# Performance work log

Measured on AMD Instinct MI355X. Metric: run time of the kernel, lower is better.

Reference implementation:

```python
import jax, jax.numpy as jnp
import numpy as np

B, S, C, H = 2, 3144, 256, 8
HD = C // H                      # head_dim = key_dim = 32
SCALE = HD ** -0.5
QN = 8                           # queriesNum hard-coded in source
KS = 5                           # lepe depthwise conv kernel


def setup_inputs() -> dict:
    key = jax.random.key(0)
    ks = jax.random.split(key, 10)
    gain_qkv = 2 ** (-2.5) * (2.0 / (C + C)) ** 0.5  # xavier_normal std with gain 2^-2.5
    gain_out = (2.0 / (C + C)) ** 0.5
    return {
        "x": jax.random.normal(ks[0], (B, S, C), jnp.float32),
        "mask": jax.random.uniform(ks[1], (B, S, S), jnp.float32),
        "wq": jax.random.normal(ks[2], (C, C), jnp.float32) * gain_qkv,
        "bq": jnp.zeros((C,), jnp.float32),
        "wk": jax.random.normal(ks[3], (C, C), jnp.float32) * gain_qkv,
        "bk": jnp.zeros((C,), jnp.float32),
        "wv": jax.random.normal(ks[4], (C, C), jnp.float32) * gain_qkv,
        "bv": jnp.zeros((C,), jnp.float32),
        "lepe_w": jax.random.normal(ks[5], (KS, KS, 1, C), jnp.float32) * 0.05,  # depthwise HWIO
        "lepe_b": jnp.zeros((C,), jnp.float32),
        "wo": jax.random.normal(ks[6], (C, C), jnp.float32) * gain_out,
        "bo": jnp.zeros((C,), jnp.float32),
        "h": 56,
        "w": 56,
    }


def _dwconv(x_nhwc, kern, bias):
    # depthwise 5x5, stride 1, padding 2 (groups = channels)
    y = jax.lax.conv_general_dilated(
        x_nhwc, kern, window_strides=(1, 1), padding=((2, 2), (2, 2)),
        dimension_numbers=("NHWC", "HWIO", "NHWC"),
        feature_group_count=x_nhwc.shape[-1])
    return y + bias


def reference(x, mask, wq, bq, wk, bk, wv, bv, lepe_w, lepe_b, wo, bo, h, w):
    b, s, c = x.shape
    q = x @ wq.T + bq
    k = (x @ wk.T + bk) * SCALE
    v = x @ wv.T + bv
    # lepe positional residual on the non-query tokens
    lepe = _dwconv(v[:, QN:].reshape(b, h, w, c), lepe_w, lepe_b).reshape(b, h * w, c)
    qh = q.reshape(b, s, H, HD).transpose(0, 2, 1, 3)   # (b, H, s, hd)
    kh = k.reshape(b, s, H, HD).transpose(0, 2, 1, 3)
    vh = kh  # faithful to source: v_h = k.reshape(...)  (scaled k used as values)
    qk = jnp.einsum("bhqd,bhkd->bhqk", qh, kh)
    qk = qk + jnp.log(mask[:, None] + 1e-6)              # isSoftMask=True path
    attn = jax.nn.softmax(qk, axis=-1)
    out = jnp.einsum("bhqk,bhkd->bhqd", attn, vh)
    out = out.transpose(0, 2, 1, 3).reshape(b, s, c)
    out = out.at[:, QN:].add(lepe)
    return out @ wo.T + bo
```

## Files before the change

### kernel.cpp

```cpp
#include <hip/hip_runtime.h>


#define S_LEN 3144
#define SP    3200
#define HEADS 8
#define HD    32
#define BATCH 2
#define MROWS (BATCH*S_LEN)
#define NPIX  3136
#define SCALE_F 0.17677669529663687f

typedef __bf16 bf16x8  __attribute__((ext_vector_type(8)));
typedef __bf16 bf16x4  __attribute__((ext_vector_type(4)));
typedef float  floatx4 __attribute__((ext_vector_type(4)));
typedef short  shortx4 __attribute__((ext_vector_type(4)));

static __device__ __forceinline__ float bf2f(unsigned int h) {
  union { unsigned int u; float f; } v; v.u = h << 16; return v.f;
}
static __device__ __forceinline__ unsigned short f2bf(float f) {
  union { __bf16 b; unsigned short u; } v; v.b = (__bf16)f; return v.u;
}
static __device__ __forceinline__ bf16x8 ldcvt8(const float* __restrict__ p) {
  float4 a = *(const float4*)p;
  float4 b = *(const float4*)(p + 4);
  bf16x8 r;
  r[0]=(__bf16)a.x; r[1]=(__bf16)a.y; r[2]=(__bf16)a.z; r[3]=(__bf16)a.w;
  r[4]=(__bf16)b.x; r[5]=(__bf16)b.y; r[6]=(__bf16)b.z; r[7]=(__bf16)b.w;
  return r;
}

#define GLOBAL_AS __attribute__((address_space(1)))
#define LDS_AS    __attribute__((address_space(3)))
static __device__ __forceinline__ void gload_lds16(const void* g, void* l) {
  __builtin_amdgcn_global_load_lds((const GLOBAL_AS void*)g, (LDS_AS void*)l, 16, 0, 0);
}

__global__ __launch_bounds__(256) void k_qkv(
    const float* __restrict__ x,
    const float* __restrict__ wqp, const float* __restrict__ bqp,
    const float* __restrict__ wkp, const float* __restrict__ bkp,
    const float* __restrict__ wvp, const float* __restrict__ bvp,
    unsigned short* __restrict__ qws, unsigned short* __restrict__ kws,
    unsigned short* __restrict__ vfrag, unsigned short* __restrict__ vstage)
{
  __shared__ unsigned short lds_t[64 * 65];
  const int lane = threadIdx.x & 63;
  const int wid  = threadIdx.x >> 6;
  const int c    = lane & 15, quad = lane >> 4;
  const int bsel  = blockIdx.x / 50;
  const int stile = blockIdx.x % 50;
  const int srow0 = stile * 64;
  const int ncol = blockIdx.y * 64;
  const int wsel = ncol >> 8;
  const int col0 = ncol & 255;

  const float* wptr = (wsel == 0) ? wqp : (wsel == 1) ? wkp : wvp;
  const float* bptr = (wsel == 0) ? bqp : (wsel == 1) ? bkp : bvp;

  const int srow = srow0 + wid * 16 + c;
  const int arow = bsel * S_LEN + ((srow < S_LEN) ? srow : 0);
  const float* ap = x    + (size_t)arow * 256 + quad * 8;
  const float* bp = wptr + (size_t)(col0 + c) * 256 + quad * 8;

  floatx4 acc[4];
#pragma unroll
  for (int ct = 0; ct < 4; ++ct) acc[ct] = (floatx4){0.f, 0.f, 0.f, 0.f};

#pragma unroll
  for (int ks = 0; ks < 8; ++ks) {
    bf16x8 af = ldcvt8(ap + ks * 32);
#pragma unroll
    for (int ct = 0; ct < 4; ++ct) {
      bf16x8 bf = ldcvt8(bp + (size_t)ct * 16 * 256 + ks * 32);
      acc[ct] = __builtin_amdgcn_mfma_f32_16x16x32_bf16(af, bf, acc[ct], 0, 0, 0);
    }
  }

#pragma unroll
  for (int ct = 0; ct < 4; ++ct) {
    const int col = col0 + ct * 16 + c;
    const float bias = bptr[col];
#pragma unroll
    for (int r = 0; r < 4; ++r) {
      const int s = srow0 + quad * 4 + r + wid * 16;
      const int valid = (s < S_LEN);
      const float v = acc[ct][r] + bias;
      if (wsel == 0) {
        qws[(((size_t)(bsel * HEADS + (col >> 5))) * SP + s) * HD + (col & 31)] =
            valid ? f2bf(v) : (unsigned short)0;
      } else if (wsel == 1) {
        const unsigned short kb16 = valid ? f2bf(v * SCALE_F) : (unsigned short)0;
        kws[(((size_t)(bsel * HEADS + (col >> 5))) * SP + s) * HD + (col & 31)] = kb16;
        lds_t[(ct * 16 + c) * 65 + (wid * 16 + quad * 4 + r)] = kb16;
      } else {
        if (valid) vstage[(size_t)(bsel * S_LEN + s) * 256 + col] = f2bf(v);
      }
    }
  }

  if (wsel == 1) {
    __syncthreads();
    const int tid = threadIdx.x;
#pragma unroll
    for (int j = 0; j < 4; ++j) {
      const int grp  = j * 4 + (tid >> 6);
      const int l    = tid & 63;
      const int ct2  = grp & 3;
      const int half = (grp >> 2) & 1;
      const int hsel = grp >> 3;
      const int cc = l & 15, qq = l >> 4;
      const int cl = hsel * 32 + half * 16 + cc;
      const int rb = ct2 * 16 + qq * 4;
      union { shortx4 s4; unsigned short u[4]; } pk;
#pragma unroll
      for (int e = 0; e < 4; ++e) pk.u[e] = lds_t[cl * 65 + rb + e];
      const int hglob = (col0 >> 5) + hsel;
      const size_t off =
          ((((size_t)(bsel * HEADS + hglob) * 50 + stile) * 4 + ct2) * 2 + half) * 64 + l;
      *(shortx4*)(vfrag + off * 4) = pk.s4;
    }
  }
}

__global__ __launch_bounds__(256) void k_lepe(const unsigned short* __restrict__ vws,
                                              const float* __restrict__ cw,
                                              const float* __restrict__ cb,
                                              unsigned short* __restrict__ lepe)
{
  int idx = blockIdx.x * 256 + threadIdx.x;
  if (idx >= BATCH * NPIX * 32) return;
  const int cg = idx & 31;
  const int p  = (idx >> 5) % NPIX;
  const int b  = idx / (NPIX * 32);
  const int y  = p / 56, xx = p - y * 56;

  float acc[8];
  {
    float4 b0 = *(const float4*)(cb + cg * 8);
    float4 b1 = *(const float4*)(cb + cg * 8 + 4);
    acc[0]=b0.x; acc[1]=b0.y; acc[2]=b0.z; acc[3]=b0.w;
    acc[4]=b1.x; acc[5]=b1.y; acc[6]=b1.z; acc[7]=b1.w;
  }
#pragma unroll
  for (int dy = -2; dy <= 2; ++dy) {
    const int yy = y + dy;
    if ((unsigned)yy >= 56u) continue;
#pragma unroll
    for (int dx = -2; dx <= 2; ++dx) {
      const int xs = xx + dx;
      if ((unsigned)xs >= 56u) continue;
      uint4 vv = *(const uint4*)(vws + (size_t)(b * S_LEN + 8 + yy * 56 + xs) * 256 + cg * 8);
      const float* wp = cw + (size_t)((dy + 2) * 5 + (dx + 2)) * 256 + cg * 8;
      float4 w0 = *(const float4*)wp;
      float4 w1 = *(const float4*)(wp + 4);
      unsigned int va[4] = {vv.x, vv.y, vv.z, vv.w};
      acc[0] += bf2f(va[0] & 0xFFFFu) * w0.x;  acc[1] += bf2f(va[0] >> 16) * w0.y;
      acc[2] += bf2f(va[1] & 0xFFFFu) * w0.z;  acc[3] += bf2f(va[1] >> 16) * w0.w;
      acc[4] += bf2f(va[2] & 0xFFFFu) * w1.x;  acc[5] += bf2f(va[2] >> 16) * w1.y;
      acc[6] += bf2f(va[3] & 0xFFFFu) * w1.z;  acc[7] += bf2f(va[3] >> 16) * w1.w;
    }
  }
  unsigned int o[4];
#pragma unroll
  for (int j = 0; j < 4; ++j)
    o[j] = (unsigned int)f2bf(acc[2*j]) | ((unsigned int)f2bf(acc[2*j+1]) << 16);
  *((uint4*)(lepe + (size_t)(b * NPIX + p) * 256 + cg * 8)) = make_uint4(o[0], o[1], o[2], o[3]);
}

template<bool TAIL>
static __device__ __forceinline__ void proc_tile(
    int t, const unsigned short* __restrict__ kb,
    const unsigned short* __restrict__ vb,
    const float* __restrict__ mb,
    int c, int quad, int lane, const bf16x8 qf,
    floatx4& o0, floatx4& o1, float& l_run)
{
  const int k0 = t * 64;
  bf16x8 kf[4]; shortx4 v0[4], v1[4];
  const unsigned short* tb = vb + (size_t)t * 2048;
#pragma unroll
  for (int ct = 0; ct < 4; ++ct) {
    kf[ct] = *(const bf16x8*)(kb + (size_t)(k0 + ct * 16 + c) * HD + quad * 8);
    v0[ct] = *(const shortx4*)(tb + (ct * 2 + 0) * 256 + lane * 4);
    v1[ct] = *(const shortx4*)(tb + (ct * 2 + 1) * 256 + lane * 4);
  }
  floatx4 s[4];
#pragma unroll
  for (int ct = 0; ct < 4; ++ct)
    s[ct] = __builtin_amdgcn_mfma_f32_16x16x32_bf16(kf[ct], qf,
               (floatx4){0.f,0.f,0.f,0.f}, 0, 0, 0);
  float ls = 0.f;
  shortx4 pf[4];
#pragma unroll
  for (int ct = 0; ct < 4; ++ct) {
    const float4 mv = *(const float4*)(mb + c * 64 + (((ct * 4 + quad) ^ c) * 4));
    float pr[4];
    pr[0] = (mv.x + 1e-6f) * __expf(s[ct][0]);
    pr[1] = (mv.y + 1e-6f) * __expf(s[ct][1]);
    pr[2] = (mv.z + 1e-6f) * __expf(s[ct][2]);
    pr[3] = (mv.w + 1e-6f) * __expf(s[ct][3]);
    if (TAIL) {
      const int kk = k0 + ct * 16 + quad * 4;
#pragma unroll
      for (int r = 0; r < 4; ++r) if (kk + r >= S_LEN) pr[r] = 0.f;
    }
    ls += (pr[0] + pr[1]) + (pr[2] + pr[3]);
    union { bf16x4 b4; shortx4 s4; } u;
    u.b4[0]=(__bf16)pr[0]; u.b4[1]=(__bf16)pr[1]; u.b4[2]=(__bf16)pr[2]; u.b4[3]=(__bf16)pr[3];
    pf[ct] = u.s4;
  }
  l_run += ls;
#pragma unroll
  for (int ct = 0; ct < 4; ++ct) {
    o0 = __builtin_amdgcn_mfma_f32_16x16x16bf16_1k(v0[ct], pf[ct], o0, 0, 0, 0);
    o1 = __builtin_amdgcn_mfma_f32_16x16x16bf16_1k(v1[ct], pf[ct], o1, 0, 0, 0);
  }
}

__global__ __launch_bounds__(256) void k_flash(
    const unsigned short* __restrict__ qws,
    const unsigned short* __restrict__ kws,
    const unsigned short* __restrict__ vfrag,
    const float* __restrict__ mask,
    const unsigned short* __restrict__ lepe,
    unsigned short* __restrict__ attn)
{
  __shared__ __align__(16) float smem[4][2048];
  const int lane = threadIdx.x & 63;
  const int wid  = threadIdx.x >> 6;
  const int c    = lane & 15, quad = lane >> 4;
  const int u    = blockIdx.x;
  const int xcd  = u & 7;
  const int slot = u >> 3;
  const int h    = slot & 7;
  const int p    = (slot >> 3) * 8 + xcd;
  const int b    = p / 200;
  const int strip = p - b * 200;
  const int qrow = strip * 16 + c;
  const size_t bh = (size_t)(b * HEADS + h);

  const bf16x8 qf = *(const bf16x8*)(qws + (bh * SP + qrow) * HD + quad * 8);
  const unsigned short* kb = kws + bh * SP * HD;
  const unsigned short* vb = vfrag + bh * (size_t)(50 * 2048);
  float* mt = &smem[wid][0];

  const float* msrc[4];
  int goff4[4];
#pragma unroll
  for (int i = 0; i < 4; ++i) {
    const int rq = i * 4 + (lane >> 4);
    int mr = strip * 16 + rq; if (mr >= S_LEN) mr = S_LEN - 1;
    msrc[i] = mask + ((size_t)b * S_LEN + mr) * S_LEN;
    goff4[i] = ((lane & 15) ^ rq) * 4;
  }

  float l_run = 0.f;
  floatx4 o0 = (floatx4){0.f,0.f,0.f,0.f};
  floatx4 o1 = (floatx4){0.f,0.f,0.f,0.f};

  const int nt = (wid < 2) ? 13 : 12;

  {
    const int k0 = (wid * 12) * 64;
#pragma unroll
    for (int i = 0; i < 4; ++i)
      gload_lds16(msrc[i] + (k0 + goff4[i]), mt + i * 256);
  }

  for (int it = 0; it < nt; ++it) {
    const int t = (it < 12) ? wid * 12 + it : 48 + wid;
    if (it + 1 < nt) {
      const int tn = (it + 1 < 12) ? wid * 12 + it + 1 : 48 + wid;
      const int k0n = tn * 64;
      float* dst = mt + ((it + 1) & 1) * 1024;
      const bool tailn = (k0n + 63 >= S_LEN);
#pragma unroll
      for (int i = 0; i < 4; ++i) {
        int kk = k0n + goff4[i];
        if (tailn && kk > S_LEN - 4) kk = S_LEN - 4;
        gload_lds16(msrc[i] + kk, dst + i * 256);
      }
      asm volatile("s_waitcnt vmcnt(4)" ::: "memory");
    } else {
      asm volatile("s_waitcnt vmcnt(0)" ::: "memory");
    }
    const float* mb = mt + (it & 1) * 1024;
    if (wid == 1 && it == 12)
      proc_tile<true >(t, kb, vb, mb, c, quad, lane, qf, o0, o1, l_run);
    else
      proc_tile<false>(t, kb, vb, mb, c, quad, lane, qf, o0, o1, l_run);
  }

#pragma unroll
  for (int r = 0; r < 4; ++r) {
    smem[wid][lane * 9 + r]     = o0[r];
    smem[wid][lane * 9 + 4 + r] = o1[r];
  }
  smem[wid][lane * 9 + 8] = l_run;
  __syncthreads();

  if (wid == 0) {
#pragma unroll
    for (int w = 1; w < 4; ++w) {
#pragma unroll
      for (int r = 0; r < 4; ++r) {
        o0[r] += smem[w][lane * 9 + r];
        o1[r] += smem[w][lane * 9 + 4 + r];
      }
      l_run += smem[w][lane * 9 + 8];
    }
    l_run += __shfl_xor(l_run, 16);
    l_run += __shfl_xor(l_run, 32);
    const float rl = 1.f / l_run;

    if (qrow < S_LEN) {
      const size_t obase = ((size_t)b * S_LEN + qrow) * 256 + h * 32;
      const size_t lbase = (qrow >= 8) ? (((size_t)b * NPIX + (qrow - 8)) * 256 + h * 32) : 0;
#pragma unroll
      for (int mt2 = 0; mt2 < 2; ++mt2) {
        floatx4 ov = mt2 ? o1 : o0;
#pragma unroll
        for (int r = 0; r < 4; ++r) {
          const int d = mt2 * 16 + quad * 4 + r;
          float val = ov[r] * rl;
          if (qrow >= 8) val += bf2f(lepe[lbase + d]);
          attn[obase + d] = f2bf(val);
        }
      }
    }
  }
}

__global__ __launch_bounds__(256) void k_oproj(
    const unsigned short* __restrict__ attn,
    const float* __restrict__ wop,
    const float* __restrict__ bop,
    float* __restrict__ out)
{
  const int lane = threadIdx.x & 63;
  const int wid  = threadIdx.x >> 6;
  const int c = lane & 15, quad = lane >> 4;
  const int row0 = blockIdx.x * 64 + wid * 16;
  const int col0 = blockIdx.y * 64;

  int arow = row0 + c; if (arow >= MROWS) arow = 0;
  const unsigned short* ap = attn + (size_t)arow * 256 + quad * 8;
  const float* bp = wop + (size_t)(col0 + c) * 256 + quad * 8;

  floatx4 acc[4];
#pragma unroll
  for (int ct = 0; ct < 4; ++ct) acc[ct] = (floatx4){0.f,0.f,0.f,0.f};
#pragma unroll
  for (int ks = 0; ks < 8; ++ks) {
    bf16x8 af = *(const bf16x8*)(ap + ks * 32);
#pragma unroll
    for (int ct = 0; ct < 4; ++ct) {
      bf16x8 bf = ldcvt8(bp + (size_t)ct * 16 * 256 + ks * 32);
      acc[ct] = __builtin_amdgcn_mfma_f32_16x16x32_bf16(af, bf, acc[ct], 0, 0, 0);
    }
  }
#pragma unroll
  for (int ct = 0; ct < 4; ++ct) {
    const int col = col0 + ct * 16 + c;
    const float bias = bop[col];
#pragma unroll
    for (int r = 0; r < 4; ++r) {
      const int row = row0 + quad * 4 + r;
      if (row >= MROWS) continue;
      out[(size_t)row * 256 + col] = acc[ct][r] + bias;
    }
  }
}

#define QW_OFF 0u
#define KW_OFF 3276800u
#define VF_OFF 6553600u
#define LE_OFF 9830400u
#define AT_OFF 13041664u

extern "C" void kernel_launch(void* const* d_in, const int* in_sizes, int n_in,
                              void* d_out, int out_size, void* d_ws, size_t ws_size,
                              hipStream_t stream) {
  const float* x    = (const float*)d_in[0];
  const float* mask = (const float*)d_in[1];
  const float* wq   = (const float*)d_in[2];
  const float* bq   = (const float*)d_in[3];
  const float* wk   = (const float*)d_in[4];
  const float* bk   = (const float*)d_in[5];
  const float* wv   = (const float*)d_in[6];
  const float* bv   = (const float*)d_in[7];
  const float* lw   = (const float*)d_in[8];
  const float* lb   = (const float*)d_in[9];
  const float* wo   = (const float*)d_in[10];
  const float* bo   = (const float*)d_in[11];

  char* ws = (char*)d_ws;
  unsigned short* qws = (unsigned short*)(ws + QW_OFF);
  unsigned short* kws = (unsigned short*)(ws + KW_OFF);
  unsigned short* vfr = (unsigned short*)(ws + VF_OFF);
  unsigned short* lpe = (unsigned short*)(ws + LE_OFF);
  unsigned short* atb = (unsigned short*)(ws + AT_OFF);
  unsigned short* vst = (unsigned short*)d_out;
  float*          outf = (float*)d_out;

  k_qkv<<<dim3(100, 12), 256, 0, stream>>>(x, wq, bq, wk, bk, wv, bv, qws, kws, vfr, vst);
  k_lepe<<<784, 256, 0, stream>>>(vst, lw, lb, lpe);
  k_flash<<<3200, 256, 0, stream>>>(qws, kws, vfr, mask, lpe, atb);
  k_oproj<<<dim3(99, 4), 256, 0, stream>>>(atb, wo, bo, outf);
}
```

Baseline: 324.5 us.

## Pre-convert inputs to bf16, double-buffer K/V registers, use exp2 in flash

Adds a conversion kernel that turns x and the QKV weights into bf16 once, so the projection GEMM loads bf16 directly instead of converting fp32 on every load. The flash kernel now double-buffers K/V fragments in registers alongside the mask tiles in LDS, reads the mask with inline ds_read_b128 asm, and requests 3 blocks per SM through launch_bounds. The K used for scores is prescaled by log2(e) so the kernel can call the exp2 builtin. This adds a kernel launch, extra workspace aliasing into the output and LDS buffers, and higher register pressure.

After: 374.8 us. +15.5%, slower.

```diff
diff --git a/kernel.cpp b/kernel.cpp
--- a/kernel.cpp
+++ b/kernel.cpp
@@ -9,6 +9,7 @@
 #define MROWS (BATCH*S_LEN)
 #define NPIX  3136
 #define SCALE_F 0.17677669529663687f
+#define KQ_SC   0.25504472665352026f
 
 typedef __bf16 bf16x8  __attribute__((ext_vector_type(8)));
 typedef __bf16 bf16x4  __attribute__((ext_vector_type(4)));
@@ -36,11 +37,36 @@
   __builtin_amdgcn_global_load_lds((const GLOBAL_AS void*)g, (LDS_AS void*)l, 16, 0, 0);
 }
 
+#define FENCE16() asm volatile("s_waitcnt vmcnt(16)" ::: "memory")
+#define FENCE0()  asm volatile("s_waitcnt vmcnt(0)" ::: "memory")
+
+__global__ __launch_bounds__(256) void k_cvt(
+    const float* __restrict__ x, const float* __restrict__ wq,
+    const float* __restrict__ wk, const float* __restrict__ wv,
+    unsigned short* __restrict__ xb, unsigned short* __restrict__ w3b)
+{
+  const int i = blockIdx.x * 256 + threadIdx.x;
+  const int NX = MROWS * 32;
+  const int NW = 8192;
+  const float* src;
+  unsigned short* dst;
+  if (i < NX) { src = x + (size_t)i * 8; dst = xb + (size_t)i * 8; }
+  else {
+    const int j = i - NX;
+    if (j >= 3 * NW) return;
+    src = (j < NW) ? wq + (size_t)j * 8
+        : (j < 2 * NW) ? wk + (size_t)(j - NW) * 8
+                       : wv + (size_t)(j - 2 * NW) * 8;
+    dst = w3b + (size_t)j * 8;
+  }
+  bf16x8 v = ldcvt8(src);
+  *(bf16x8*)dst = v;
+}
+
 __global__ __launch_bounds__(256) void k_qkv(
-    const float* __restrict__ x,
-    const float* __restrict__ wqp, const float* __restrict__ bqp,
-    const float* __restrict__ wkp, const float* __restrict__ bkp,
-    const float* __restrict__ wvp, const float* __restrict__ bvp,
+    const unsigned short* __restrict__ xb, const unsigned short* __restrict__ w3b,
+    const float* __restrict__ bqp, const float* __restrict__ bkp,
+    const float* __restrict__ bvp,
     unsigned short* __restrict__ qws, unsigned short* __restrict__ kws,
     unsigned short* __restrict__ vfrag, unsigned short* __restrict__ vstage)
 {
@@ -55,13 +81,12 @@
   const int wsel = ncol >> 8;
   const int col0 = ncol & 255;
 
-  const float* wptr = (wsel == 0) ? wqp : (wsel == 1) ? wkp : wvp;
   const float* bptr = (wsel == 0) ? bqp : (wsel == 1) ? bkp : bvp;
 
   const int srow = srow0 + wid * 16 + c;
   const int arow = bsel * S_LEN + ((srow < S_LEN) ? srow : 0);
-  const float* ap = x    + (size_t)arow * 256 + quad * 8;
-  const float* bp = wptr + (size_t)(col0 + c) * 256 + quad * 8;
+  const unsigned short* ap = xb  + (size_t)arow * 256 + quad * 8;
+  const unsigned short* bp = w3b + (size_t)(ncol + c) * 256 + quad * 8;
 
   floatx4 acc[4];
 #pragma unroll
@@ -69,10 +94,10 @@
 
 #pragma unroll
   for (int ks = 0; ks < 8; ++ks) {
-    bf16x8 af = ldcvt8(ap + ks * 32);
+    bf16x8 af = *(const bf16x8*)(ap + ks * 32);
 #pragma unroll
     for (int ct = 0; ct < 4; ++ct) {
-      bf16x8 bf = ldcvt8(bp + (size_t)ct * 16 * 256 + ks * 32);
+      bf16x8 bf = *(const bf16x8*)(bp + (size_t)ct * 16 * 256 + ks * 32);
       acc[ct] = __builtin_amdgcn_mfma_f32_16x16x32_bf16(af, bf, acc[ct], 0, 0, 0);
     }
   }
@@ -83,16 +108,17 @@
     const float bias = bptr[col];
 #pragma unroll
     for (int r = 0; r < 4; ++r) {
-      const int s = srow0 + quad * 4 + r + wid * 16;
+      const int s = srow0 + wid * 16 + quad * 4 + r;
       const int valid = (s < S_LEN);
       const float v = acc[ct][r] + bias;
       if (wsel == 0) {
         qws[(((size_t)(bsel * HEADS + (col >> 5))) * SP + s) * HD + (col & 31)] =
             valid ? f2bf(v) : (unsigned short)0;
       } else if (wsel == 1) {
-        const unsigned short kb16 = valid ? f2bf(v * SCALE_F) : (unsigned short)0;
-        kws[(((size_t)(bsel * HEADS + (col >> 5))) * SP + s) * HD + (col & 31)] = kb16;
-        lds_t[(ct * 16 + c) * 65 + (wid * 16 + quad * 4 + r)] = kb16;
+        kws[(((size_t)(bsel * HEADS + (col >> 5))) * SP + s) * HD + (col & 31)] =
+            valid ? f2bf(v * KQ_SC) : (unsigned short)0;
+        lds_t[(ct * 16 + c) * 65 + (wid * 16 + quad * 4 + r)] =
+            valid ? f2bf(v * SCALE_F) : (unsigned short)0;
       } else {
         if (valid) vstage[(size_t)(bsel * S_LEN + s) * 256 + col] = f2bf(v);
       }
@@ -168,16 +194,26 @@
   *((uint4*)(lepe + (size_t)(b * NPIX + p) * 256 + cg * 8)) = make_uint4(o[0], o[1], o[2], o[3]);
 }
 
-template<bool TAIL>
-static __device__ __forceinline__ void proc_tile(
-    int t, const unsigned short* __restrict__ kb,
-    const unsigned short* __restrict__ vb,
-    const float* __restrict__ mb,
-    int c, int quad, int lane, const bf16x8 qf,
-    floatx4& o0, floatx4& o1, float& l_run)
+
+static __device__ __forceinline__ void ldsm4(
+    const unsigned (&ma)[4], floatx4& m0, floatx4& m1, floatx4& m2, floatx4& m3)
+{
+  asm volatile(
+      "ds_read_b128 %0, %4\n\t"
+      "ds_read_b128 %1, %5\n\t"
+      "ds_read_b128 %2, %6\n\t"
+      "ds_read_b128 %3, %7\n\t"
+      "s_waitcnt lgkmcnt(0)"
+      : "=v"(m0), "=v"(m1), "=v"(m2), "=v"(m3)
+      : "v"(ma[0]), "v"(ma[1]), "v"(ma[2]), "v"(ma[3]));
+}
+
+static __device__ __forceinline__ void load_reg(
+    const unsigned short* __restrict__ kb, const unsigned short* __restrict__ vb,
+    int t, int c, int quad, int lane,
+    bf16x8 (&kf)[4], shortx4 (&v0)[4], shortx4 (&v1)[4])
 {
   const int k0 = t * 64;
-  bf16x8 kf[4]; shortx4 v0[4], v1[4];
   const unsigned short* tb = vb + (size_t)t * 2048;
 #pragma unroll
   for (int ct = 0; ct < 4; ++ct) {
@@ -185,21 +221,49 @@
     v0[ct] = *(const shortx4*)(tb + (ct * 2 + 0) * 256 + lane * 4);
     v1[ct] = *(const shortx4*)(tb + (ct * 2 + 1) * 256 + lane * 4);
   }
+}
+
+static __device__ __forceinline__ void stage_mask(
+    const float* const (&msrc)[4], const int (&goff4)[4], int k0, float* dst)
+{
+#pragma unroll
+  for (int i = 0; i < 4; ++i)
+    gload_lds16(msrc[i] + (k0 + goff4[i]), dst + i * 256);
+}
+
+static __device__ __forceinline__ void stage_mask_tail(
+    const float* const (&msrc)[4], const int (&goff4)[4], int k0, float* dst)
+{
+#pragma unroll
+  for (int i = 0; i < 4; ++i) {
+    int kk = k0 + goff4[i];
+    if (kk > S_LEN - 4) kk = S_LEN - 4;
+    gload_lds16(msrc[i] + kk, dst + i * 256);
+  }
+}
+
+template<bool TAIL>
+static __device__ __forceinline__ void proc_reg(
+    int k0, const bf16x8 (&kf)[4], const shortx4 (&v0)[4], const shortx4 (&v1)[4],
+    const unsigned (&ma)[4], int quad, const bf16x8 qf,
+    floatx4& o0, floatx4& o1, float& l_run)
+{
   floatx4 s[4];
 #pragma unroll
   for (int ct = 0; ct < 4; ++ct)
     s[ct] = __builtin_amdgcn_mfma_f32_16x16x32_bf16(kf[ct], qf,
                (floatx4){0.f,0.f,0.f,0.f}, 0, 0, 0);
+  floatx4 mv0, mv1, mv2, mv3;
+  ldsm4(ma, mv0, mv1, mv2, mv3);
+  const floatx4 mv[4] = {mv0, mv1, mv2, mv3};
   float ls = 0.f;
   shortx4 pf[4];
 #pragma unroll
   for (int ct = 0; ct < 4; ++ct) {
-    const float4 mv = *(const float4*)(mb + c * 64 + (((ct * 4 + quad) ^ c) * 4));
     float pr[4];
-    pr[0] = (mv.x + 1e-6f) * __expf(s[ct][0]);
-    pr[1] = (mv.y + 1e-6f) * __expf(s[ct][1]);
-    pr[2] = (mv.z + 1e-6f) * __expf(s[ct][2]);
-    pr[3] = (mv.w + 1e-6f) * __expf(s[ct][3]);
+#pragma unroll
+    for (int r = 0; r < 4; ++r)
+      pr[r] = (mv[ct][r] + 1e-6f) * __builtin_amdgcn_exp2f(s[ct][r]);
     if (TAIL) {
       const int kk = k0 + ct * 16 + quad * 4;
 #pragma unroll
@@ -218,7 +282,7 @@
   }
 }
 
-__global__ __launch_bounds__(256) void k_flash(
+__global__ __launch_bounds__(256, 3) void k_flash(
     const unsigned short* __restrict__ qws,
     const unsigned short* __restrict__ kws,
     const unsigned short* __restrict__ vfrag,
@@ -245,6 +309,16 @@
   const unsigned short* vb = vfrag + bh * (size_t)(50 * 2048);
   float* mt = &smem[wid][0];
 
+  unsigned au[4], ad[4];
+  {
+    const unsigned base = (unsigned)(size_t)(LDS_AS void*)&smem[wid][0];
+#pragma unroll
+    for (int ct = 0; ct < 4; ++ct) {
+      au[ct] = base + (unsigned)((c * 64 + (((ct * 4 + quad) ^ c) & 15) * 4) * 4);
+      ad[ct] = au[ct] + 4096u;
+    }
+  }
+
   const float* msrc[4];
   int goff4[4];
 #pragma unroll
@@ -259,37 +333,43 @@
   floatx4 o0 = (floatx4){0.f,0.f,0.f,0.f};
   floatx4 o1 = (floatx4){0.f,0.f,0.f,0.f};
 
-  const int nt = (wid < 2) ? 13 : 12;
-
-  {
-    const int k0 = (wid * 12) * 64;
-#pragma unroll
-    for (int i = 0; i < 4; ++i)
-      gload_lds16(msrc[i] + (k0 + goff4[i]), mt + i * 256);
-  }
-
-  for (int it = 0; it < nt; ++it) {
-    const int t = (it < 12) ? wid * 12 + it : 48 + wid;
-    if (it + 1 < nt) {
-      const int tn = (it + 1 < 12) ? wid * 12 + it + 1 : 48 + wid;
-      const int k0n = tn * 64;
-      float* dst = mt + ((it + 1) & 1) * 1024;
-      const bool tailn = (k0n + 63 >= S_LEN);
-#pragma unroll
-      for (int i = 0; i < 4; ++i) {
-        int kk = k0n + goff4[i];
-        if (tailn && kk > S_LEN - 4) kk = S_LEN - 4;
-        gload_lds16(msrc[i] + kk, dst + i * 256);
-      }
-      asm volatile("s_waitcnt vmcnt(4)" ::: "memory");
+  const int tbase = wid * 12;
+  bf16x8 kfA[4], kfB[4];
+  shortx4 v0A[4], v1A[4], v0B[4], v1B[4];
+
+  stage_mask(msrc, goff4, tbase * 64, mt);
+  load_reg(kb, vb, tbase, c, quad, lane, kfA, v0A, v1A);
+
+#pragma unroll 1
+  for (int itp = 0; itp < 6; ++itp) {
+    const int j0 = 2 * itp;
+    load_reg(kb, vb, tbase + j0 + 1, c, quad, lane, kfB, v0B, v1B);
+    stage_mask(msrc, goff4, (tbase + j0 + 1) * 64, mt + 1024);
+    FENCE16();
+    proc_reg<false>(0, kfA, v0A, v1A, au, quad, qf, o0, o1, l_run);
+    if (itp < 5) {
+      load_reg(kb, vb, tbase + j0 + 2, c, quad, lane, kfA, v0A, v1A);
+      stage_mask(msrc, goff4, (tbase + j0 + 2) * 64, mt);
+      FENCE16();
+    } else if (wid == 0) {
+      load_reg(kb, vb, 48, c, quad, lane, kfA, v0A, v1A);
+      stage_mask(msrc, goff4, 48 * 64, mt);
+      FENCE16();
+    } else if (wid == 1) {
+      load_reg(kb, vb, 49, c, quad, lane, kfA, v0A, v1A);
+      stage_mask_tail(msrc, goff4, 49 * 64, mt);
+      FENCE16();
     } else {
-      asm volatile("s_waitcnt vmcnt(0)" ::: "memory");
-    }
-    const float* mb = mt + (it & 1) * 1024;
-    if (wid == 1 && it == 12)
-      proc_tile<true >(t, kb, vb, mb, c, quad, lane, qf, o0, o1, l_run);
-    else
-      proc_tile<false>(t, kb, vb, mb, c, quad, lane, qf, o0, o1, l_run);
+      FENCE0();
+    }
+    proc_reg<false>(0, kfB, v0B, v1B, ad, quad, qf, o0, o1, l_run);
+  }
+  if (wid == 0) {
+    FENCE0();
+    proc_reg<false>(0, kfA, v0A, v1A, au, quad, qf, o0, o1, l_run);
+  } else if (wid == 1) {
+    FENCE0();
+    proc_reg<true>(49 * 64, kfA, v0A, v1A, au, quad, qf, o0, o1, l_run);
   }
 
 #pragma unroll
@@ -399,12 +479,15 @@
   unsigned short* qws = (unsigned short*)(ws + QW_OFF);
   unsigned short* kws = (unsigned short*)(ws + KW_OFF);
   unsigned short* vfr = (unsigned short*)(ws + VF_OFF);
+  unsigned short* w3b = (unsigned short*)(ws + LE_OFF);
   unsigned short* lpe = (unsigned short*)(ws + LE_OFF);
   unsigned short* atb = (unsigned short*)(ws + AT_OFF);
   unsigned short* vst = (unsigned short*)d_out;
+  unsigned short* xb  = (unsigned short*)d_out + 1609728;
   float*          outf = (float*)d_out;
 
-  k_qkv<<<dim3(100, 12), 256, 0, stream>>>(x, wq, bq, wk, bk, wv, bv, qws, kws, vfr, vst);
+  k_cvt<<<882, 256, 0, stream>>>(x, wq, wk, wv, xb, w3b);
+  k_qkv<<<dim3(100, 12), 256, 0, stream>>>(xb, w3b, bq, bk, bv, qws, kws, vfr, vst);
   k_lepe<<<784, 256, 0, stream>>>(vst, lw, lb, lpe);
   k_flash<<<3200, 256, 0, stream>>>(qws, kws, vfr, mask, lpe, atb);
   k_oproj<<<dim3(99, 4), 256, 0, stream>>>(atb, wo, bo, outf);
```
